# Optimization experiments

Measured on AMD Instinct MI355X. Metric: run time of the kernel, lower is better.

## Reference

```python
import jax, jax.numpy as jnp
import numpy as np

jax.config.update("jax_enable_x64", True)

# Dims (see shape_source): batch, heads, q-len, kv-len, head-channels, quant group
B, H, T, S, HC = 2, 16, 1024, 1024, 128
G = 8            # group_size from A/R_QUANT_PARAMS
SCALE_SHIFT = 14 # combined dequant shift applied to integer QK scores before softmax
O_SM = 14        # fixed-point offset of the integer softmax output (LUT-style)
PROB_QMAX = 255.0  # 8-bit unsigned probability mantissa (R_QUANT_PARAMS n_bits=8)


def _dequant_po2(q, s):
    """q: int mantissas [..., N], s: nonneg po2 shift exponents [..., N//G].
    Emulates (q << s) per group of G channels (pot_scale activation quantizer)."""
    s_full = jnp.repeat(s, G, axis=-1)
    return q.astype(jnp.float64) * jnp.exp2(s_full.astype(jnp.float64))


def setup_inputs() -> dict:
    key = jax.random.key(0)
    ks = jax.random.split(key, 6)
    # signed 8-bit mantissas in [-128, 127]
    q_q = jax.random.randint(ks[0], (B, H, T, HC), 0, 256, dtype=jnp.int32) - 128
    k_q = jax.random.randint(ks[1], (B, H, S, HC), 0, 256, dtype=jnp.int32) - 128
    vt_q = jax.random.randint(ks[2], (B, H, HC, S), 0, 256, dtype=jnp.int32) - 128
    # nonnegative power-of-two shifts, one per group of G=8
    q_s = jax.random.randint(ks[3], (B, H, T, HC // G), 0, 4, dtype=jnp.int32)
    k_s = jax.random.randint(ks[4], (B, H, S, HC // G), 0, 4, dtype=jnp.int32)
    vt_s = jax.random.randint(ks[5], (B, H, HC, S // G), 0, 4, dtype=jnp.int32)
    return {"q_q": q_q, "q_s": q_s, "k_q": k_q, "k_s": k_s, "vt_q": vt_q, "vt_s": vt_s}


def reference(q_q, q_s, k_q, k_s, vt_q, vt_s):
    # ---- shift_qk_matmul: (q_q << q_s) @ (k_q << k_s)^T in float64, truncated to int64
    q = _dequant_po2(q_q, q_s)                       # [B,H,T,HC] f64
    k = _dequant_po2(k_q, k_s)                       # [B,H,S,HC] f64
    scores = jnp.einsum("bhtc,bhsc->bhts", q, k).astype(jnp.int64)

    # ---- integer softmax emulation: rescale integer scores, softmax, then
    # re-quantize probabilities with an 8-bit per-group (G=8 along S) po2 scale
    logits = scores.astype(jnp.float32) * np.float32(2.0 ** (-SCALE_SHIFT) / np.sqrt(HC))
    p = jax.nn.softmax(logits, axis=-1)              # [B,H,T,S]
    val = jnp.round(p * (2.0 ** O_SM))               # fixed-point probs (ints)
    vg = val.reshape(B, H, T, S // G, G)
    gmax = jnp.max(vg, axis=-1, keepdims=True)
    r_shift = jnp.clip(jnp.ceil(jnp.log2(jnp.maximum(gmax, 1.0) / PROB_QMAX)), 0.0, None)
    r_q = jnp.clip(jnp.round(vg / jnp.exp2(r_shift)), 0.0, PROB_QMAX)
    r = (r_q * jnp.exp2(r_shift)).reshape(B, H, T, S).astype(jnp.float64)  # (r_q << r_s)

    # ---- shift_rv_matmul: r @ (vt_q << vt_s)^T in float64, truncated to int64
    vt = _dequant_po2(vt_q, vt_s)                    # [B,H,HC,S] f64
    a = jnp.einsum("bhts,bhcs->bhtc", r, vt).astype(jnp.int64)  # [B,H,T,HC]
    return a
```

## Files before the change

### kernel.cpp

```cpp
#include <hip/hip_runtime.h>
#include <string.h>


typedef int   v4i __attribute__((ext_vector_type(4)));
typedef float v4f __attribute__((ext_vector_type(4)));
typedef short v8s __attribute__((ext_vector_type(8)));
typedef unsigned v2u __attribute__((ext_vector_type(2)));

#define BHN 32
#define TN  1024
#define SN  1024
#define HCN 128
#define TT  32
#define KD_BH 262144
#define VD_BH 262144
#define WS_NEED ((size_t)BHN*(KD_BH+VD_BH))

__device__ __forceinline__ unsigned pack_b(int b0,int b1,int b2,int b3){
    return (unsigned)((b0&255)|((b1&255)<<8)|((b2&255)<<16)|((b3&255)<<24));
}

__device__ __forceinline__ void dig16(const int* __restrict__ p, int s0, int s1,
                                      v4i& hi, v4i& lo){
    #pragma unroll
    for (int wi=0; wi<4; ++wi){
        v4i m = *(const v4i*)(p + wi*4);
        int s = (wi<2) ? s0 : s1;
        int d0=m[0]<<s, d1=m[1]<<s, d2=m[2]<<s, d3=m[3]<<s;
        hi[wi] = (int)pack_b(d0>>4,d1>>4,d2>>4,d3>>4);
        lo[wi] = (int)pack_b(d0&15,d1&15,d2&15,d3&15);
    }
}

__device__ __forceinline__ unsigned short bf16_of_int(int v){
    return (unsigned short)(__float_as_uint((float)v) >> 16);
}

__global__ __launch_bounds__(256) void digitize(
    const int* __restrict__ k_q, const int* __restrict__ k_s,
    const int* __restrict__ vt_q, const int* __restrict__ vt_s,
    unsigned char* __restrict__ kd, unsigned char* __restrict__ vd)
{
    const int w    = threadIdx.x >> 6;
    const int lane = threadIdx.x & 63;
    const int l15  = lane & 15;
    const int task = blockIdx.x*4 + w;
    if (task < 4096){
        const int kc = task & 1, n = (task>>1)&7, ch = (task>>4)&7, bh = task>>7;
        const int q4   = lane >> 4;
        const int srow = bh*SN + ch*128 + n*16 + l15;
        const int gb   = srow*16 + kc*8 + q4*2;
        v4i hi, lo;
        dig16(k_q + (size_t)srow*HCN + kc*64 + q4*16, k_s[gb], k_s[gb+1], hi, lo);
        size_t base = (size_t)bh*KD_BH + (size_t)(ch*32768 + n*4096 + kc*2048 + lane*16);
        *(v4i*)(kd + base)        = hi;
        *(v4i*)(kd + base + 1024) = lo;
    } else {
        const int t  = task - 4096;
        const int n  = t & 7, kb = (t>>3)&31, bh = t>>8;
        const int sub = lane >> 4;
        const int row = bh*HCN + n*16 + l15;
        const int* vp = vt_q + (size_t)row*SN + kb*32 + sub*8;
        const int s   = vt_s[row*128 + kb*4 + sub];
        unsigned wds[4];
        #pragma unroll
        for (int j=0;j<4;j++){
            int a = vp[j*2]   << s;
            int b = vp[j*2+1] << s;
            wds[j] = (unsigned)bf16_of_int(a) | ((unsigned)bf16_of_int(b) << 16);
        }
        size_t base = (size_t)bh*VD_BH + (size_t)(((kb*8 + n)*64 + lane)*16);
        *(v4i*)(vd + base) = v4i{(int)wds[0],(int)wds[1],(int)wds[2],(int)wds[3]};
    }
}

template<bool PK>
__global__ __launch_bounds__(256,2) void mha_mfma(
    const int* __restrict__ q_q, const int* __restrict__ q_s,
    const int* __restrict__ k_q, const int* __restrict__ k_s,
    const int* __restrict__ vt_q, const int* __restrict__ vt_s,
    const unsigned char* __restrict__ kd, const unsigned char* __restrict__ vd,
    int* __restrict__ out)
{
    __shared__ __align__(16) unsigned short rbuf[32*1024];
    __shared__ float red[256];

    const int tid  = threadIdx.x;
    const int ln   = tid & 15;
    const int qd4  = (tid >> 4) & 3;
    const int w    = tid >> 6;
    const int lane = tid & 63;
    const int blk = blockIdx.x;
    const int bh  = ((blk>>8)<<3) | (blk&7);
    const int t0  = ((blk>>3)&31) * TT;

    v4i qfh[2][2], qfl[2][2];
    #pragma unroll
    for (int h=0; h<2; ++h){
        const int* qrow  = q_q + (size_t)(bh*TN + t0 + h*16 + ln)*HCN;
        const int* qsrow = q_s + (size_t)(bh*TN + t0 + h*16 + ln)*16;
        #pragma unroll
        for (int kc=0; kc<2; ++kc){
            int gi = kc*8 + qd4*2;
            dig16(qrow + kc*64 + qd4*16, qsrow[gi], qsrow[gi+1], qfh[h][kc], qfl[h][kc]);
        }
    }

    int scv[2][16][4];

    const v4i* kb_ = (const v4i*)(kd + (size_t)bh*KD_BH);
    #pragma unroll
    for (int ch=0; ch<8; ++ch){
        #pragma unroll
        for (int i=0;i<2;i++){
            const int n = w*2 + i;
            v4i a2[2]={{0,0,0,0},{0,0,0,0}}, a1[2]={{0,0,0,0},{0,0,0,0}},
                a0[2]={{0,0,0,0},{0,0,0,0}};
            #pragma unroll
            for (int kc=0;kc<2;kc++){
                v4i bhv, blv;
                if (PK){
                    const v4i* tb = kb_ + (ch*8+n)*256 + kc*128 + lane;
                    bhv = tb[0];
                    blv = tb[64];
                } else {
                    int srow = bh*SN + ch*128 + n*16 + ln;
                    int cc   = kc*64 + qd4*16;
                    dig16(k_q + (size_t)srow*128 + cc,
                          k_s[srow*16 + (cc>>3)], k_s[srow*16 + (cc>>3) + 1], bhv, blv);
                }
                #pragma unroll
                for (int h=0;h<2;h++){
                    a2[h] = __builtin_amdgcn_mfma_i32_16x16x64_i8(bhv, qfh[h][kc], a2[h], 0,0,0);
                    a1[h] = __builtin_amdgcn_mfma_i32_16x16x64_i8(bhv, qfl[h][kc], a1[h], 0,0,0);
                    a1[h] = __builtin_amdgcn_mfma_i32_16x16x64_i8(blv, qfh[h][kc], a1[h], 0,0,0);
                    a0[h] = __builtin_amdgcn_mfma_i32_16x16x64_i8(blv, qfl[h][kc], a0[h], 0,0,0);
                }
            }
            int st = ch*2 + i;
            #pragma unroll
            for (int h=0;h<2;h++)
                #pragma unroll
                for (int r=0;r<4;r++)
                    scv[h][st][r] = (a2[h][r]<<8) + (a1[h][r]<<4) + a0[h][r];
        }
    }

    const float CS2 = (float)(6.103515625e-05 / 11.313708498984760390566
                              * 1.4426950408889634074);
    #pragma unroll
    for (int h=0;h<2;h++){
        float m0=-3.0e38f, m1=-3.0e38f, m2=-3.0e38f, m3=-3.0e38f;
        #pragma unroll
        for (int st=0;st<16;st++){
            float f0 = (float)scv[h][st][0]*CS2; scv[h][st][0]=__float_as_int(f0); m0=fmaxf(m0,f0);
            float f1 = (float)scv[h][st][1]*CS2; scv[h][st][1]=__float_as_int(f1); m1=fmaxf(m1,f1);
            float f2 = (float)scv[h][st][2]*CS2; scv[h][st][2]=__float_as_int(f2); m2=fmaxf(m2,f2);
            float f3 = (float)scv[h][st][3]*CS2; scv[h][st][3]=__float_as_int(f3); m3=fmaxf(m3,f3);
        }
        float m_ = fmaxf(fmaxf(m0,m1), fmaxf(m2,m3));
        m_ = fmaxf(m_, __shfl_xor(m_, 16));
        m_ = fmaxf(m_, __shfl_xor(m_, 32));
        if ((tid & 48) == 0) red[h*64 + w*16 + ln] = m_;
    }
    __syncthreads();
    float inv14[2];
    #pragma unroll
    for (int h=0;h<2;h++){
        const float mrow = fmaxf(fmaxf(red[h*64+ln], red[h*64+16+ln]),
                                 fmaxf(red[h*64+32+ln], red[h*64+48+ln]));
        float s0=0.f, s1=0.f, s2=0.f, s3=0.f;
        #pragma unroll
        for (int st=0;st<16;st++){
            #pragma unroll
            for (int r=0;r<4;r++){
                float t_ = __int_as_float(scv[h][st][r]) - mrow;
                float e;
                asm("v_exp_f32 %0, %1" : "=v"(e) : "v"(t_));
                scv[h][st][r] = __float_as_int(e);
                if (r==0) s0 += e; else if (r==1) s1 += e; else if (r==2) s2 += e; else s3 += e;
            }
        }
        float s_ = (s0+s1) + (s2+s3);
        s_ += __shfl_xor(s_, 16);
        s_ += __shfl_xor(s_, 32);
        if ((tid & 48) == 0) red[128 + h*64 + w*16 + ln] = s_;
    }
    __syncthreads();
    #pragma unroll
    for (int h=0;h<2;h++){
        float sum = red[128+h*64+ln] + red[128+h*64+16+ln]
                  + red[128+h*64+32+ln] + red[128+h*64+48+ln];
        inv14[h] = 16384.0f / sum;
    }

    {
        const int lnr = ln & 7;
        const int cbase = w*32 + qd4*4;
        #pragma unroll
        for (int h=0;h<2;h++){
            unsigned short* rp = rbuf + (h*16 + ln)*1024;
            #pragma unroll
            for (int st=0;st<16;st++){
                float v0 = rintf(__int_as_float(scv[h][st][0]) * inv14[h]);
                float v1 = rintf(__int_as_float(scv[h][st][1]) * inv14[h]);
                float v2 = rintf(__int_as_float(scv[h][st][2]) * inv14[h]);
                float v3 = rintf(__int_as_float(scv[h][st][3]) * inv14[h]);
                float g = fmaxf(fmaxf(v0,v1), fmaxf(v2,v3));
                g = fmaxf(g, __shfl_xor(g, 16));
                int gi = max((int)g, 1);
                int x  = gi - 1;
                int e2 = 31 - __clz(x | 255);
                int sh = (e2 - 7) + ((x >> (e2 - 7)) == 255);
                float isc = __int_as_float((127 - sh) << 23);
                float fsc = __int_as_float((127 + sh) << 23);
                unsigned b0 = __float_as_uint(rintf(v0*isc) * fsc);
                unsigned b1 = __float_as_uint(rintf(v1*isc) * fsc);
                unsigned b2 = __float_as_uint(rintf(v2*isc) * fsc);
                unsigned b3 = __float_as_uint(rintf(v3*isc) * fsc);
                unsigned w0 = __builtin_amdgcn_perm(b1, b0, 0x07060302u);
                unsigned w1 = __builtin_amdgcn_perm(b3, b2, 0x07060302u);
                int c0 = (st>>1)*128 + cbase + (st&1)*16;
                int g_ = c0 >> 3;
                int gs = (g_ & 0x78) | ((g_ + lnr) & 7);
                *(v2u*)(rp + gs*8 + (c0&7)) = v2u{w0, w1};
            }
        }
    }
    __syncthreads();

    const v4i* vb = (const v4i*)(vd + (size_t)bh*VD_BH);
    const unsigned short* rp0 = rbuf + ln*1024;
    const unsigned short* rp1 = rbuf + (16 + ln)*1024;
    const int lnr2 = ln & 7;
    v4f acc00{0,0,0,0}, acc01{0,0,0,0}, acc10{0,0,0,0}, acc11{0,0,0,0};
    #pragma unroll 4
    for (int kb=0; kb<32; ++kb){
        int g2  = kb*4 + qd4;
        int gs2 = (g2 & 0x78) | ((g2 + lnr2) & 7);
        v8s af0 = *(const v8s*)(rp0 + gs2*8);
        v8s af1 = *(const v8s*)(rp1 + gs2*8);
        v4i b0, b1;
        if (PK){
            b0 = vb[(kb*8 + w*2    )*64 + lane];
            b1 = vb[(kb*8 + w*2 + 1)*64 + lane];
        } else {
            #pragma unroll
            for (int i=0;i<2;i++){
                int chan = (w*2+i)*16 + ln;
                const int* vp = vt_q + (size_t)(bh*HCN + chan)*SN + kb*32 + qd4*8;
                int s = vt_s[(bh*HCN + chan)*128 + kb*4 + qd4];
                unsigned wd[4];
                #pragma unroll
                for (int j=0;j<4;j++){
                    int a = vp[j*2]   << s;
                    int b = vp[j*2+1] << s;
                    wd[j] = (unsigned)bf16_of_int(a) | ((unsigned)bf16_of_int(b)<<16);
                }
                v4i t{(int)wd[0],(int)wd[1],(int)wd[2],(int)wd[3]};
                if (i==0) b0 = t; else b1 = t;
            }
        }
        v8s bs0, bs1;
        memcpy(&bs0, &b0, 16);
        memcpy(&bs1, &b1, 16);
        acc00 = __builtin_amdgcn_mfma_f32_16x16x32_bf16(af0, bs0, acc00, 0,0,0);
        acc01 = __builtin_amdgcn_mfma_f32_16x16x32_bf16(af0, bs1, acc01, 0,0,0);
        acc10 = __builtin_amdgcn_mfma_f32_16x16x32_bf16(af1, bs0, acc10, 0,0,0);
        acc11 = __builtin_amdgcn_mfma_f32_16x16x32_bf16(af1, bs1, acc11, 0,0,0);
    }
    #pragma unroll
    for (int r=0;r<4;r++){
        size_t o0 = (size_t)(bh*TN + t0 + qd4*4 + r)*HCN + w*32 + ln;
        out[o0]      = (int)rintf(acc00[r]);
        out[o0 + 16] = (int)rintf(acc01[r]);
        size_t o1 = o0 + (size_t)16*HCN;
        out[o1]      = (int)rintf(acc10[r]);
        out[o1 + 16] = (int)rintf(acc11[r]);
    }
}

extern "C" void kernel_launch(void* const* d_in, const int* in_sizes, int n_in,
                              void* d_out, int out_size, void* d_ws, size_t ws_size,
                              hipStream_t stream) {
    const int* q_q  = (const int*)d_in[0];
    const int* q_s  = (const int*)d_in[1];
    const int* k_q  = (const int*)d_in[2];
    const int* k_s  = (const int*)d_in[3];
    const int* vt_q = (const int*)d_in[4];
    const int* vt_s = (const int*)d_in[5];
    int* out = (int*)d_out;

    unsigned char* kd = (unsigned char*)d_ws;
    unsigned char* vd = kd + (size_t)BHN*KD_BH;

    if (ws_size >= WS_NEED){
        digitize<<<dim3(3072), 256, 0, stream>>>(k_q,k_s,vt_q,vt_s, kd,vd);
        mha_mfma<true><<<dim3(1024), 256, 0, stream>>>(
            q_q,q_s,k_q,k_s,vt_q,vt_s, kd,vd, out);
    } else {
        mha_mfma<false><<<dim3(1024), 256, 0, stream>>>(
            q_q,q_s,k_q,k_s,vt_q,vt_s, kd,vd, out);
    }
}
```

Before: 176.8 us.

## Double block to 512 threads, halve per-wave work, integer max, padded LDS rows

Each block now runs 8 waves instead of 4, so every wave handles one 16-column S tile per chunk and one 16-channel output tile. This halves the per-thread score registers and is meant to raise latency hiding. The row max is now taken on the integer scores before scaling, which saves a multiply per element in that pass. The XOR-swizzled probability buffer is replaced by rows padded to 1032 elements to avoid bank conflicts. Each Q fragment is now computed by twice as many waves, the reductions span 8 waves, and LDS use grows slightly.

```diff
diff --git a/kernel.cpp b/kernel.cpp
--- a/kernel.cpp
+++ b/kernel.cpp
@@ -12,6 +12,7 @@
 #define SN  1024
 #define HCN 128
 #define TT  32
+#define RST 1032
 #define KD_BH 262144
 #define VD_BH 262144
 #define WS_NEED ((size_t)BHN*(KD_BH+VD_BH))
@@ -75,15 +76,16 @@
 }
 
 template<bool PK>
-__global__ __launch_bounds__(256,2) void mha_mfma(
+__global__ __launch_bounds__(512,2) void mha_mfma(
     const int* __restrict__ q_q, const int* __restrict__ q_s,
     const int* __restrict__ k_q, const int* __restrict__ k_s,
     const int* __restrict__ vt_q, const int* __restrict__ vt_s,
     const unsigned char* __restrict__ kd, const unsigned char* __restrict__ vd,
     int* __restrict__ out)
 {
-    __shared__ __align__(16) unsigned short rbuf[32*1024];
-    __shared__ float red[256];
+    __shared__ __align__(16) unsigned short rbuf[32*RST];
+    __shared__ int   redi[256];
+    __shared__ float redf[256];
 
     const int tid  = threadIdx.x;
     const int ln   = tid & 15;
@@ -106,177 +108,154 @@
         }
     }
 
-    int scv[2][16][4];
+    int scv[2][8][4];
 
     const v4i* kb_ = (const v4i*)(kd + (size_t)bh*KD_BH);
     #pragma unroll
     for (int ch=0; ch<8; ++ch){
-        #pragma unroll
-        for (int i=0;i<2;i++){
-            const int n = w*2 + i;
-            v4i a2[2]={{0,0,0,0},{0,0,0,0}}, a1[2]={{0,0,0,0},{0,0,0,0}},
-                a0[2]={{0,0,0,0},{0,0,0,0}};
-            #pragma unroll
-            for (int kc=0;kc<2;kc++){
-                v4i bhv, blv;
-                if (PK){
-                    const v4i* tb = kb_ + (ch*8+n)*256 + kc*128 + lane;
-                    bhv = tb[0];
-                    blv = tb[64];
-                } else {
-                    int srow = bh*SN + ch*128 + n*16 + ln;
-                    int cc   = kc*64 + qd4*16;
-                    dig16(k_q + (size_t)srow*128 + cc,
-                          k_s[srow*16 + (cc>>3)], k_s[srow*16 + (cc>>3) + 1], bhv, blv);
-                }
-                #pragma unroll
-                for (int h=0;h<2;h++){
-                    a2[h] = __builtin_amdgcn_mfma_i32_16x16x64_i8(bhv, qfh[h][kc], a2[h], 0,0,0);
-                    a1[h] = __builtin_amdgcn_mfma_i32_16x16x64_i8(bhv, qfl[h][kc], a1[h], 0,0,0);
-                    a1[h] = __builtin_amdgcn_mfma_i32_16x16x64_i8(blv, qfh[h][kc], a1[h], 0,0,0);
-                    a0[h] = __builtin_amdgcn_mfma_i32_16x16x64_i8(blv, qfl[h][kc], a0[h], 0,0,0);
-                }
-            }
-            int st = ch*2 + i;
-            #pragma unroll
-            for (int h=0;h<2;h++)
-                #pragma unroll
-                for (int r=0;r<4;r++)
-                    scv[h][st][r] = (a2[h][r]<<8) + (a1[h][r]<<4) + a0[h][r];
-        }
+        v4i a2[2]={{0,0,0,0},{0,0,0,0}}, a1[2]={{0,0,0,0},{0,0,0,0}},
+            a0[2]={{0,0,0,0},{0,0,0,0}};
+        #pragma unroll
+        for (int kc=0;kc<2;kc++){
+            v4i bhv, blv;
+            if (PK){
+                const v4i* tb = kb_ + (ch*8+w)*256 + kc*128 + lane;
+                bhv = tb[0];
+                blv = tb[64];
+            } else {
+                int srow = bh*SN + ch*128 + w*16 + ln;
+                int cc   = kc*64 + qd4*16;
+                dig16(k_q + (size_t)srow*128 + cc,
+                      k_s[srow*16 + (cc>>3)], k_s[srow*16 + (cc>>3) + 1], bhv, blv);
+            }
+            #pragma unroll
+            for (int h=0;h<2;h++){
+                a2[h] = __builtin_amdgcn_mfma_i32_16x16x64_i8(bhv, qfh[h][kc], a2[h], 0,0,0);
+                a1[h] = __builtin_amdgcn_mfma_i32_16x16x64_i8(bhv, qfl[h][kc], a1[h], 0,0,0);
+                a1[h] = __builtin_amdgcn_mfma_i32_16x16x64_i8(blv, qfh[h][kc], a1[h], 0,0,0);
+                a0[h] = __builtin_amdgcn_mfma_i32_16x16x64_i8(blv, qfl[h][kc], a0[h], 0,0,0);
+            }
+        }
+        #pragma unroll
+        for (int h=0;h<2;h++)
+            #pragma unroll
+            for (int r=0;r<4;r++)
+                scv[h][ch][r] = (a2[h][r]<<8) + (a1[h][r]<<4) + a0[h][r];
     }
 
     const float CS2 = (float)(6.103515625e-05 / 11.313708498984760390566
                               * 1.4426950408889634074);
     #pragma unroll
     for (int h=0;h<2;h++){
-        float m0=-3.0e38f, m1=-3.0e38f, m2=-3.0e38f, m3=-3.0e38f;
-        #pragma unroll
-        for (int st=0;st<16;st++){
-            float f0 = (float)scv[h][st][0]*CS2; scv[h][st][0]=__float_as_int(f0); m0=fmaxf(m0,f0);
-            float f1 = (float)scv[h][st][1]*CS2; scv[h][st][1]=__float_as_int(f1); m1=fmaxf(m1,f1);
-            float f2 = (float)scv[h][st][2]*CS2; scv[h][st][2]=__float_as_int(f2); m2=fmaxf(m2,f2);
-            float f3 = (float)scv[h][st][3]*CS2; scv[h][st][3]=__float_as_int(f3); m3=fmaxf(m3,f3);
-        }
-        float m_ = fmaxf(fmaxf(m0,m1), fmaxf(m2,m3));
-        m_ = fmaxf(m_, __shfl_xor(m_, 16));
-        m_ = fmaxf(m_, __shfl_xor(m_, 32));
-        if ((tid & 48) == 0) red[h*64 + w*16 + ln] = m_;
+        int m0=-2147483647, m1=-2147483647, m2=-2147483647, m3=-2147483647;
+        #pragma unroll
+        for (int ch=0;ch<8;ch++){
+            m0 = max(m0, scv[h][ch][0]);
+            m1 = max(m1, scv[h][ch][1]);
+            m2 = max(m2, scv[h][ch][2]);
+            m3 = max(m3, scv[h][ch][3]);
+        }
+        int m_ = max(max(m0,m1), max(m2,m3));
+        m_ = max(m_, __shfl_xor(m_, 16));
+        m_ = max(m_, __shfl_xor(m_, 32));
+        if (qd4 == 0) redi[h*128 + w*16 + ln] = m_;
     }
     __syncthreads();
-    float inv14[2];
-    #pragma unroll
-    for (int h=0;h<2;h++){
-        const float mrow = fmaxf(fmaxf(red[h*64+ln], red[h*64+16+ln]),
-                                 fmaxf(red[h*64+32+ln], red[h*64+48+ln]));
+    #pragma unroll
+    for (int h=0;h<2;h++){
+        int mr = redi[h*128 + ln];
+        #pragma unroll
+        for (int w2=1;w2<8;w2++) mr = max(mr, redi[h*128 + w2*16 + ln]);
         float s0=0.f, s1=0.f, s2=0.f, s3=0.f;
         #pragma unroll
-        for (int st=0;st<16;st++){
+        for (int ch=0;ch<8;ch++){
             #pragma unroll
             for (int r=0;r<4;r++){
-                float t_ = __int_as_float(scv[h][st][r]) - mrow;
+                float t_ = (float)(scv[h][ch][r] - mr) * CS2;
                 float e;
                 asm("v_exp_f32 %0, %1" : "=v"(e) : "v"(t_));
-                scv[h][st][r] = __float_as_int(e);
+                scv[h][ch][r] = __float_as_int(e);
                 if (r==0) s0 += e; else if (r==1) s1 += e; else if (r==2) s2 += e; else s3 += e;
             }
         }
         float s_ = (s0+s1) + (s2+s3);
         s_ += __shfl_xor(s_, 16);
         s_ += __shfl_xor(s_, 32);
-        if ((tid & 48) == 0) red[128 + h*64 + w*16 + ln] = s_;
+        if (qd4 == 0) redf[h*128 + w*16 + ln] = s_;
     }
     __syncthreads();
-    #pragma unroll
-    for (int h=0;h<2;h++){
-        float sum = red[128+h*64+ln] + red[128+h*64+16+ln]
-                  + red[128+h*64+32+ln] + red[128+h*64+48+ln];
+    float inv14[2];
+    #pragma unroll
+    for (int h=0;h<2;h++){
+        float sum = 0.f;
+        #pragma unroll
+        for (int w2=0;w2<8;w2++) sum += redf[h*128 + w2*16 + ln];
         inv14[h] = 16384.0f / sum;
     }
 
-    {
-        const int lnr = ln & 7;
-        const int cbase = w*32 + qd4*4;
-        #pragma unroll
-        for (int h=0;h<2;h++){
-            unsigned short* rp = rbuf + (h*16 + ln)*1024;
-            #pragma unroll
-            for (int st=0;st<16;st++){
-                float v0 = rintf(__int_as_float(scv[h][st][0]) * inv14[h]);
-                float v1 = rintf(__int_as_float(scv[h][st][1]) * inv14[h]);
-                float v2 = rintf(__int_as_float(scv[h][st][2]) * inv14[h]);
-                float v3 = rintf(__int_as_float(scv[h][st][3]) * inv14[h]);
-                float g = fmaxf(fmaxf(v0,v1), fmaxf(v2,v3));
-                g = fmaxf(g, __shfl_xor(g, 16));
-                int gi = max((int)g, 1);
-                int x  = gi - 1;
-                int e2 = 31 - __clz(x | 255);
-                int sh = (e2 - 7) + ((x >> (e2 - 7)) == 255);
-                float isc = __int_as_float((127 - sh) << 23);
-                float fsc = __int_as_float((127 + sh) << 23);
-                unsigned b0 = __float_as_uint(rintf(v0*isc) * fsc);
-                unsigned b1 = __float_as_uint(rintf(v1*isc) * fsc);
-                unsigned b2 = __float_as_uint(rintf(v2*isc) * fsc);
-                unsigned b3 = __float_as_uint(rintf(v3*isc) * fsc);
-                unsigned w0 = __builtin_amdgcn_perm(b1, b0, 0x07060302u);
-                unsigned w1 = __builtin_amdgcn_perm(b3, b2, 0x07060302u);
-                int c0 = (st>>1)*128 + cbase + (st&1)*16;
-                int g_ = c0 >> 3;
-                int gs = (g_ & 0x78) | ((g_ + lnr) & 7);
-                *(v2u*)(rp + gs*8 + (c0&7)) = v2u{w0, w1};
-            }
+    #pragma unroll
+    for (int h=0;h<2;h++){
+        unsigned short* rp = rbuf + (h*16 + ln)*RST;
+        #pragma unroll
+        for (int ch=0;ch<8;ch++){
+            float v0 = rintf(__int_as_float(scv[h][ch][0]) * inv14[h]);
+            float v1 = rintf(__int_as_float(scv[h][ch][1]) * inv14[h]);
+            float v2 = rintf(__int_as_float(scv[h][ch][2]) * inv14[h]);
+            float v3 = rintf(__int_as_float(scv[h][ch][3]) * inv14[h]);
+            float g = fmaxf(fmaxf(v0,v1), fmaxf(v2,v3));
+            g = fmaxf(g, __shfl_xor(g, 16));
+            int gi = max((int)g, 1);
+            int x  = gi - 1;
+            int e2 = 31 - __clz(x | 255);
+            int sh = (e2 - 7) + ((x >> (e2 - 7)) == 255);
+            float isc = __int_as_float((127 - sh) << 23);
+            float fsc = __int_as_float((127 + sh) << 23);
+            unsigned b0 = __float_as_uint(rintf(v0*isc) * fsc);
+            unsigned b1 = __float_as_uint(rintf(v1*isc) * fsc);
+            unsigned b2 = __float_as_uint(rintf(v2*isc) * fsc);
+            unsigned b3 = __float_as_uint(rintf(v3*isc) * fsc);
+            unsigned w0 = __builtin_amdgcn_perm(b1, b0, 0x07060302u);
+            unsigned w1 = __builtin_amdgcn_perm(b3, b2, 0x07060302u);
+            int c0 = (ch*8 + w)*16 + qd4*4;
+            *(v2u*)(rp + c0) = v2u{w0, w1};
         }
     }
     __syncthreads();
 
     const v4i* vb = (const v4i*)(vd + (size_t)bh*VD_BH);
-    const unsigned short* rp0 = rbuf + ln*1024;
-    const unsigned short* rp1 = rbuf + (16 + ln)*1024;
-    const int lnr2 = ln & 7;
-    v4f acc00{0,0,0,0}, acc01{0,0,0,0}, acc10{0,0,0,0}, acc11{0,0,0,0};
+    const unsigned short* rp0 = rbuf + ln*RST;
+    const unsigned short* rp1 = rbuf + (16 + ln)*RST;
+    v4f acc0{0,0,0,0}, acc1{0,0,0,0};
     #pragma unroll 4
     for (int kb=0; kb<32; ++kb){
-        int g2  = kb*4 + qd4;
-        int gs2 = (g2 & 0x78) | ((g2 + lnr2) & 7);
-        v8s af0 = *(const v8s*)(rp0 + gs2*8);
-        v8s af1 = *(const v8s*)(rp1 + gs2*8);
-        v4i b0, b1;
+        v8s af0 = *(const v8s*)(rp0 + kb*32 + qd4*8);
+        v8s af1 = *(const v8s*)(rp1 + kb*32 + qd4*8);
+        v4i b0;
         if (PK){
-            b0 = vb[(kb*8 + w*2    )*64 + lane];
-            b1 = vb[(kb*8 + w*2 + 1)*64 + lane];
+            b0 = vb[(kb*8 + w)*64 + lane];
         } else {
-            #pragma unroll
-            for (int i=0;i<2;i++){
-                int chan = (w*2+i)*16 + ln;
-                const int* vp = vt_q + (size_t)(bh*HCN + chan)*SN + kb*32 + qd4*8;
-                int s = vt_s[(bh*HCN + chan)*128 + kb*4 + qd4];
-                unsigned wd[4];
-                #pragma unroll
-                for (int j=0;j<4;j++){
-                    int a = vp[j*2]   << s;
-                    int b = vp[j*2+1] << s;
-                    wd[j] = (unsigned)bf16_of_int(a) | ((unsigned)bf16_of_int(b)<<16);
-                }
-                v4i t{(int)wd[0],(int)wd[1],(int)wd[2],(int)wd[3]};
-                if (i==0) b0 = t; else b1 = t;
-            }
-        }
-        v8s bs0, bs1;
+            int chan = w*16 + ln;
+            const int* vp = vt_q + (size_t)(bh*HCN + chan)*SN + kb*32 + qd4*8;
+            int s = vt_s[(bh*HCN + chan)*128 + kb*4 + qd4];
+            unsigned wd[4];
+            #pragma unroll
+            for (int j=0;j<4;j++){
+                int a = vp[j*2]   << s;
+                int b = vp[j*2+1] << s;
+                wd[j] = (unsigned)bf16_of_int(a) | ((unsigned)bf16_of_int(b)<<16);
+            }
+            b0 = v4i{(int)wd[0],(int)wd[1],(int)wd[2],(int)wd[3]};
+        }
+        v8s bs0;
         memcpy(&bs0, &b0, 16);
-        memcpy(&bs1, &b1, 16);
-        acc00 = __builtin_amdgcn_mfma_f32_16x16x32_bf16(af0, bs0, acc00, 0,0,0);
-        acc01 = __builtin_amdgcn_mfma_f32_16x16x32_bf16(af0, bs1, acc01, 0,0,0);
-        acc10 = __builtin_amdgcn_mfma_f32_16x16x32_bf16(af1, bs0, acc10, 0,0,0);
-        acc11 = __builtin_amdgcn_mfma_f32_16x16x32_bf16(af1, bs1, acc11, 0,0,0);
+        acc0 = __builtin_amdgcn_mfma_f32_16x16x32_bf16(af0, bs0, acc0, 0,0,0);
+        acc1 = __builtin_amdgcn_mfma_f32_16x16x32_bf16(af1, bs0, acc1, 0,0,0);
     }
     #pragma unroll
     for (int r=0;r<4;r++){
-        size_t o0 = (size_t)(bh*TN + t0 + qd4*4 + r)*HCN + w*32 + ln;
-        out[o0]      = (int)rintf(acc00[r]);
-        out[o0 + 16] = (int)rintf(acc01[r]);
-        size_t o1 = o0 + (size_t)16*HCN;
-        out[o1]      = (int)rintf(acc10[r]);
-        out[o1 + 16] = (int)rintf(acc11[r]);
+        size_t o0 = (size_t)(bh*TN + t0 + qd4*4 + r)*HCN + w*16 + ln;
+        out[o0] = (int)rintf(acc0[r]);
+        out[o0 + (size_t)16*HCN] = (int)rintf(acc1[r]);
     }
 }
 
@@ -296,10 +275,10 @@
 
     if (ws_size >= WS_NEED){
         digitize<<<dim3(3072), 256, 0, stream>>>(k_q,k_s,vt_q,vt_s, kd,vd);
-        mha_mfma<true><<<dim3(1024), 256, 0, stream>>>(
+        mha_mfma<true><<<dim3(1024), 512, 0, stream>>>(
             q_q,q_s,k_q,k_s,vt_q,vt_s, kd,vd, out);
     } else {
-        mha_mfma<false><<<dim3(1024), 256, 0, stream>>>(
+        mha_mfma<false><<<dim3(1024), 512, 0, stream>>>(
             q_q,q_s,k_q,k_s,vt_q,vt_s, kd,vd, out);
     }
 }
```

Result: faster. 171.3 us (-3.1%).
